# Kernel optimization log

Hardware: AMD Instinct MI355X
Metric: run time of the kernel (lower is better)

## Reference

```python
import jax, jax.numpy as jnp
import numpy as np

SEQ, B, N, F_IN = 128, 32, 1024, 16
NHID, G_FEAT, H = 2, 4, 256


def setup_inputs() -> dict:
    key = jax.random.key(0)
    ks = jax.random.split(key, 14)
    inp = {}
    inp['x'] = jax.random.normal(ks[0], (SEQ, B, N, F_IN), jnp.float32)
    # row-scaled random dense adjacency (keeps activations well-conditioned)
    inp['adj'] = jax.random.uniform(ks[1], (N, N), jnp.float32) * (1.0 / N)
    inp['gc1_w'] = jax.random.normal(ks[2], (F_IN, NHID), jnp.float32) * 0.3
    inp['gc1_b'] = jax.random.normal(ks[3], (NHID,), jnp.float32) * 0.1
    inp['gc2_w'] = jax.random.normal(ks[4], (NHID, G_FEAT), jnp.float32) * 0.3
    inp['gc2_b'] = jax.random.normal(ks[5], (G_FEAT,), jnp.float32) * 0.1
    in0 = G_FEAT * N  # GRU layer-0 input size = G_feat * num_nodes
    inp['w_ih_l0'] = jax.random.normal(ks[6], (3 * H, in0), jnp.float32) * 0.02
    inp['w_hh_l0'] = jax.random.normal(ks[7], (3 * H, H), jnp.float32) * 0.05
    inp['b_ih_l0'] = jax.random.normal(ks[8], (3 * H,), jnp.float32) * 0.05
    inp['b_hh_l0'] = jax.random.normal(ks[9], (3 * H,), jnp.float32) * 0.05
    inp['w_ih_l1'] = jax.random.normal(ks[10], (3 * H, H), jnp.float32) * 0.05
    inp['w_hh_l1'] = jax.random.normal(ks[11], (3 * H, H), jnp.float32) * 0.05
    inp['b_ih_l1'] = jax.random.normal(ks[12], (3 * H,), jnp.float32) * 0.05
    inp['b_hh_l1'] = jax.random.normal(ks[13], (3 * H,), jnp.float32) * 0.05
    return inp


def gru_layer(x_seq, h0, w_ih, w_hh, b_ih, b_hh):
    # torch nn.GRU gate math, gate order (r, z, n)
    def step(h, x_t):
        gi = x_t @ w_ih.T + b_ih          # (B, 3H)
        gh = h @ w_hh.T + b_hh            # (B, 3H)
        i_r, i_z, i_n = jnp.split(gi, 3, axis=-1)
        h_r, h_z, h_n = jnp.split(gh, 3, axis=-1)
        r = jax.nn.sigmoid(i_r + h_r)
        z = jax.nn.sigmoid(i_z + h_z)
        n = jnp.tanh(i_n + r * h_n)
        h_new = (1.0 - z) * n + z * h
        return h_new, h_new
    hT, out = jax.lax.scan(step, h0, x_seq)
    return out, hT


def reference(x, adj, gc1_w, gc1_b, gc2_w, gc2_b,
              w_ih_l0, w_hh_l0, b_ih_l0, b_hh_l0,
              w_ih_l1, w_hh_l1, b_ih_l1, b_hh_l1):
    # GCN, vectorized over (seq, batch). GraphConvolution: adj @ (x @ W) + b
    s = jnp.einsum('sbnf,fh->sbnh', x, gc1_w) + gc1_b
    s = jnp.einsum('mn,sbnh->sbmh', adj, s)
    s = jax.nn.relu(s)
    # dropout inactive in eval mode
    s = jnp.einsum('sbnh,hg->sbng', s, gc2_w) + gc2_b
    s = jnp.einsum('mn,sbng->sbmg', adj, s)
    s = jax.nn.log_softmax(s, axis=2)  # dim=1 of per-step (B, N, G) == node axis
    out = s.reshape(SEQ, B, N * G_FEAT)  # .view(batch, -1) per step, stacked
    h0 = jnp.zeros((B, H), out.dtype)
    out, h1 = gru_layer(out, h0, w_ih_l0, w_hh_l0, b_ih_l0, b_hh_l0)
    out, h2 = gru_layer(out, h0, w_ih_l1, w_hh_l1, b_ih_l1, b_hh_l1)
    hn = jnp.stack([h1, h2])  # (n_layers, B, H)
    return out, hn
```

## Files before the change

### kernel.cpp

```cpp
#include <hip/hip_runtime.h>
#include <stdint.h>

constexpr int SEQL = 128;
constexpr int BAT  = 32;
constexpr int NN   = 1024;
constexpr int FIN  = 16;
constexpr int HH   = 256;
constexpr int PQ   = SEQL * BAT;
constexpr float LSM_SHIFT = 6.9314718055994531f;

using f32x4 = __attribute__((ext_vector_type(4))) float;
using s16x8 = __attribute__((ext_vector_type(8))) short;
using u32x4 = __attribute__((ext_vector_type(4))) unsigned int;

__device__ __forceinline__ unsigned short f2bf(float x) {
  unsigned u = __float_as_uint(x);
  u += 0x7fffu + ((u >> 16) & 1u);
  return (unsigned short)(u >> 16);
}
__device__ __forceinline__ float sigm(float x) { return 1.f / (1.f + __expf(-x)); }

__device__ __forceinline__ void gl_lds16(const void* g, void* l) {
  __builtin_amdgcn_global_load_lds(
      (const __attribute__((address_space(1))) void*)g,
      (__attribute__((address_space(3))) void*)l, 16, 0, 0);
}

#if __has_builtin(__builtin_amdgcn_fdot2_f32_bf16)
typedef __bf16 bf16x2_t __attribute__((ext_vector_type(2)));
__device__ __forceinline__ float dot2bf(unsigned w, unsigned h, float acc) {
  return __builtin_amdgcn_fdot2_f32_bf16(__builtin_bit_cast(bf16x2_t, w),
                                         __builtin_bit_cast(bf16x2_t, h), acc, false);
}
#else
__device__ __forceinline__ float dot2bf(unsigned w, unsigned h, float acc) {
  acc += __uint_as_float(w << 16) * __uint_as_float(h << 16);
  acc += __uint_as_float(w & 0xffff0000u) * __uint_as_float(h & 0xffff0000u);
  return acc;
}
#endif

__global__ __launch_bounds__(256) void k1_xw1(const float* __restrict__ x,
    const float* __restrict__ w1, const float* __restrict__ b1,
    unsigned short* __restrict__ Yt) {
  int idx = blockIdx.x * 256 + threadIdx.x;
  int p = idx >> 10, n = idx & 1023;
  const float* xp = x + (size_t)idx * FIN;
  float xv[16];
  *(float4*)(xv + 0)  = *(const float4*)(xp + 0);
  *(float4*)(xv + 4)  = *(const float4*)(xp + 4);
  *(float4*)(xv + 8)  = *(const float4*)(xp + 8);
  *(float4*)(xv + 12) = *(const float4*)(xp + 12);
  float y0 = b1[0], y1 = b1[1];
#pragma unroll
  for (int f = 0; f < 16; ++f) { y0 += xv[f] * w1[2*f]; y1 += xv[f] * w1[2*f+1]; }
  Yt[(size_t)(2*p)   * NN + n] = f2bf(y0);
  Yt[(size_t)(2*p+1) * NN + n] = f2bf(y1);
}

__global__ __launch_bounds__(256) void k_cvt(const float* __restrict__ in,
    unsigned short* __restrict__ out, int n4) {
  int i = blockIdx.x * 256 + threadIdx.x;
  if (i >= n4) return;
  float4 v = *(const float4*)(in + (size_t)i * 4);
  ushort4 o;
  o.x = f2bf(v.x); o.y = f2bf(v.y); o.z = f2bf(v.z); o.w = f2bf(v.w);
  *(ushort4*)(out + (size_t)i * 4) = o;
}

__global__ __launch_bounds__(256) void k_biasadj(const float* __restrict__ wih0,
    const float* __restrict__ bih0, float* __restrict__ biasAdj) {
  int wid = threadIdx.x >> 6, lane = threadIdx.x & 63;
  int j = blockIdx.x * 4 + wid;
  const float* row = wih0 + (size_t)j * 4096;
  float s = 0.f;
  for (int k = lane * 4; k < 4096; k += 256) {
    float4 v = *(const float4*)(row + k);
    s += v.x + v.y + v.z + v.w;
  }
#pragma unroll
  for (int off = 32; off >= 1; off >>= 1) s += __shfl_xor(s, off);
  if (lane == 0) biasAdj[j] = bih0[j] - LSM_SHIFT * s;
}

template <int KS>
__global__ __launch_bounds__(256) void k_prep(const float* __restrict__ W,
    unsigned* __restrict__ Wp) {
  int tid = blockIdx.x * 256 + threadIdx.x;
  int j = tid >> 7, k2 = tid & 127;
  float2 wv = *(const float2*)(W + (size_t)j * 256 + 2 * k2);
  unsigned pk = (unsigned)f2bf(wv.x) | ((unsigned)f2bf(wv.y) << 16);
  int i = j >> 8, jg = j & 255;
  if (KS == 4) {
    int kg = k2 >> 5, c = (k2 >> 2) & 7, u = k2 & 3;
    Wp[(((i * 4 + kg) * 8 + c) << 10) + (jg << 2) + u] = pk;
  } else {
    int kg = k2 >> 6, c = (k2 >> 2) & 15, u = k2 & 3;
    Wp[(((i * 2 + kg) * 16 + c) << 10) + (jg << 2) + u] = pk;
  }
}

template <int EPI>
__global__ __launch_bounds__(256) void gemm_bt(
    const unsigned short* __restrict__ A, const unsigned short* __restrict__ B,
    void* __restrict__ Cout, const float* __restrict__ bias, int K, int ldc) {
  __shared__ __align__(16) unsigned short As[128 * 64];
  __shared__ __align__(16) unsigned short Bs[128 * 64];
  const int tid = threadIdx.x;
  const int lane = tid & 63, wave = tid >> 6;
  const int ln15 = lane & 15, hi4 = lane >> 4;
  const int wr = wave >> 1, wc = wave & 1;
  const int m0 = blockIdx.y * 128, n0 = blockIdx.x * 128;
  const int rsub = lane >> 3, csub = lane & 7;

  f32x4 acc[4][4];
#pragma unroll
  for (int i = 0; i < 4; ++i)
#pragma unroll
    for (int j = 0; j < 4; ++j) acc[i][j] = {0.f, 0.f, 0.f, 0.f};

  for (int kt = 0; kt < K; kt += 64) {
    __syncthreads();
#pragma unroll
    for (int j = 0; j < 4; ++j) {
      int qq = wave * 4 + j;
      const unsigned short* ga = A + (size_t)(m0 + qq*8 + rsub) * K + kt + csub*8;
      gl_lds16(ga, &As[qq * 512]);
      const unsigned short* gb = B + (size_t)(n0 + qq*8 + rsub) * K + kt + csub*8;
      gl_lds16(gb, &Bs[qq * 512]);
    }
    __syncthreads();
#pragma unroll
    for (int kk = 0; kk < 2; ++kk) {
      s16x8 af[4], bfr[4];
#pragma unroll
      for (int mi = 0; mi < 4; ++mi)
        af[mi] = *(const s16x8*)&As[(wr*64 + mi*16 + ln15) * 64 + kk*32 + hi4*8];
#pragma unroll
      for (int ni = 0; ni < 4; ++ni)
        bfr[ni] = *(const s16x8*)&Bs[(wc*64 + ni*16 + ln15) * 64 + kk*32 + hi4*8];
#pragma unroll
      for (int mi = 0; mi < 4; ++mi)
#pragma unroll
        for (int ni = 0; ni < 4; ++ni)
          acc[mi][ni] = __builtin_amdgcn_mfma_f32_16x16x32_bf16(
              af[mi], bfr[ni], acc[mi][ni], 0, 0, 0);
    }
  }

  if (EPI == 2) {
    float* C = (float*)Cout;
#pragma unroll
    for (int ni = 0; ni < 4; ++ni) {
      int j = n0 + wc*64 + ni*16 + ln15;
      float bv = bias[j];
#pragma unroll
      for (int mi = 0; mi < 4; ++mi) {
        int m = m0 + wr*64 + mi*16 + hi4*4;
#pragma unroll
        for (int r = 0; r < 4; ++r) C[(size_t)(m + r) * ldc + j] = acc[mi][ni][r] + bv;
      }
    }
  } else {
    unsigned short* C = (unsigned short*)Cout;
#pragma unroll
    for (int ni = 0; ni < 4; ++ni) {
      int j = n0 + wc*64 + ni*16 + ln15;
#pragma unroll
      for (int mi = 0; mi < 4; ++mi) {
        int m = m0 + wr*64 + mi*16 + hi4*4;
        ushort4 v;
        float f0 = acc[mi][ni][0], f1 = acc[mi][ni][1], f2 = acc[mi][ni][2], f3 = acc[mi][ni][3];
        if (EPI == 0) { f0 = fmaxf(f0, 0.f); f1 = fmaxf(f1, 0.f); f2 = fmaxf(f2, 0.f); f3 = fmaxf(f3, 0.f); }
        v.x = f2bf(f0); v.y = f2bf(f1); v.z = f2bf(f2); v.w = f2bf(f3);
        *(ushort4*)&C[(size_t)j * ldc + m] = v;
      }
    }
  }
}

__device__ __forceinline__ unsigned k4_proc(unsigned a, unsigned b, float w0, float w1, float bb) {
  float a0 = __uint_as_float(a << 16), a1 = __uint_as_float(a & 0xffff0000u);
  float b0 = __uint_as_float(b << 16), b1 = __uint_as_float(b & 0xffff0000u);
  float y0 = a0 * w0 + b0 * w1 + bb;
  float y1 = a1 * w0 + b1 * w1 + bb;
  return (unsigned)f2bf(y0) | ((unsigned)f2bf(y1) << 16);
}

__global__ __launch_bounds__(256) void k4_w2(const unsigned short* __restrict__ z1t,
    const float* __restrict__ w2, const float* __restrict__ b2,
    unsigned short* __restrict__ Y2t) {
  int idx = blockIdx.x * 256 + threadIdx.x;
  int j4 = idx >> 7, mb = idx & 127;
  int p = j4 >> 2, g = j4 & 3;
  const unsigned short* r0 = z1t + (size_t)(p * 2) * NN + mb * 8;
  const unsigned short* r1 = r0 + NN;
  float w0 = w2[g], w1v = w2[4 + g], bb = b2[g];
  uint4 ua = *(const uint4*)r0;
  uint4 ub = *(const uint4*)r1;
  uint4 o;
  o.x = k4_proc(ua.x, ub.x, w0, w1v, bb);
  o.y = k4_proc(ua.y, ub.y, w0, w1v, bb);
  o.z = k4_proc(ua.z, ub.z, w0, w1v, bb);
  o.w = k4_proc(ua.w, ub.w, w0, w1v, bb);
  *(uint4*)(Y2t + (size_t)j4 * NN + mb * 8) = o;
}

__global__ __launch_bounds__(256) void k6_lsm(const unsigned short* __restrict__ z2t,
    unsigned short* __restrict__ Xg) {
  int wid = threadIdx.x >> 6, lane = threadIdx.x & 63;
  int r = blockIdx.x * 4 + wid;
  int p = r >> 2, g = r & 3;
  const unsigned short* row = z2t + (size_t)r * NN;
  uint4 u0 = *(const uint4*)(row + lane * 16);
  uint4 u1 = *(const uint4*)(row + lane * 16 + 8);
  unsigned uu[8] = {u0.x, u0.y, u0.z, u0.w, u1.x, u1.y, u1.z, u1.w};
  float v[16];
#pragma unroll
  for (int q = 0; q < 8; ++q) {
    v[2*q]   = __uint_as_float(uu[q] << 16);
    v[2*q+1] = __uint_as_float(uu[q] & 0xffff0000u);
  }
  float mx = v[0];
#pragma unroll
  for (int e = 1; e < 16; ++e) mx = fmaxf(mx, v[e]);
#pragma unroll
  for (int off = 32; off >= 1; off >>= 1) mx = fmaxf(mx, __shfl_xor(mx, off));
  float s = 0.f;
#pragma unroll
  for (int e = 0; e < 16; ++e) s += __expf(v[e] - mx);
#pragma unroll
  for (int off = 32; off >= 1; off >>= 1) s += __shfl_xor(s, off);
  float lse = __logf(s) + mx;
  unsigned short* xr = Xg + (size_t)p * 4096;
#pragma unroll
  for (int e = 0; e < 16; ++e) xr[(lane * 16 + e) * 4 + g] = f2bf(v[e] - lse + LSM_SHIFT);
}

template <int L>
__global__ __attribute__((amdgpu_flat_work_group_size(1024, 1024),
                          amdgpu_waves_per_eu(4, 4)))
void k_rnn4(const float* __restrict__ gi,
    const unsigned* __restrict__ Wp, const float* __restrict__ bhh,
    unsigned short* __restrict__ hb_out, float* __restrict__ hf_out,
    float* __restrict__ hn_row) {
  const int b = blockIdx.x, tid = threadIdx.x;
  const int jg = tid & 255, kg = tid >> 8;
  __shared__ __align__(16) unsigned hpk[128];
  __shared__ float part[4][776];

  unsigned w[3][8][4];
#pragma unroll
  for (int i = 0; i < 3; ++i)
#pragma unroll
    for (int c = 0; c < 8; ++c) {
      u32x4 t = *(const u32x4*)(Wp + ((((i * 4 + kg) * 8 + c) << 10) + (jg << 2)));
      w[i][c][0] = t.x; w[i][c][1] = t.y; w[i][c][2] = t.z; w[i][c][3] = t.w;
#pragma unroll
      for (int u = 0; u < 4; ++u) asm volatile("" : "+v"(w[i][c][u]));
    }

  float hprev = 0.f;
  float br = 0.f, bz = 0.f, bn = 0.f;
  float g0 = 0.f, g1 = 0.f, g2 = 0.f;
  if (tid < 256) {
    br = bhh[jg]; bz = bhh[256 + jg]; bn = bhh[512 + jg];
    const float* gr = gi + (size_t)b * 768;
    g0 = gr[jg]; g1 = gr[256 + jg]; g2 = gr[512 + jg];
  }
  if (tid < 128) hpk[tid] = 0u;
  __syncthreads();

  for (int t = 0; t < SEQL; ++t) {
    float p0 = 0.f, p1 = 0.f, p2 = 0.f;
    if (tid < 256) {
      int tt = t + 1 < SEQL ? t + 1 : SEQL - 1;
      const float* gr = gi + (size_t)(tt * BAT + b) * 768;
      p0 = gr[jg]; p1 = gr[256 + jg]; p2 = gr[512 + jg];
    }
    float a0 = 0.f, a1 = 0.f, a2 = 0.f;
    u32x4 hk = *(const u32x4*)&hpk[kg * 32];
#pragma unroll
    for (int c = 0; c < 8; ++c) {
      u32x4 hnx = (c < 7) ? *(const u32x4*)&hpk[kg * 32 + (c + 1) * 4] : hk;
      a0 = dot2bf(w[0][c][0], hk.x, a0); a0 = dot2bf(w[0][c][1], hk.y, a0);
      a0 = dot2bf(w[0][c][2], hk.z, a0); a0 = dot2bf(w[0][c][3], hk.w, a0);
      a1 = dot2bf(w[1][c][0], hk.x, a1); a1 = dot2bf(w[1][c][1], hk.y, a1);
      a1 = dot2bf(w[1][c][2], hk.z, a1); a1 = dot2bf(w[1][c][3], hk.w, a1);
      a2 = dot2bf(w[2][c][0], hk.x, a2); a2 = dot2bf(w[2][c][1], hk.y, a2);
      a2 = dot2bf(w[2][c][2], hk.z, a2); a2 = dot2bf(w[2][c][3], hk.w, a2);
      hk = hnx;
    }
    part[kg][jg]       = a0;
    part[kg][256 + jg] = a1;
    part[kg][512 + jg] = a2;
    __syncthreads();
    if (tid < 256) {
      float ghr = part[0][jg]       + part[1][jg]       + part[2][jg]       + part[3][jg]       + br;
      float ghz = part[0][256 + jg] + part[1][256 + jg] + part[2][256 + jg] + part[3][256 + jg] + bz;
      float ghn = part[0][512 + jg] + part[1][512 + jg] + part[2][512 + jg] + part[3][512 + jg] + bn;
      float r = sigm(g0 + ghr);
      float z = sigm(g1 + ghz);
      float nn = tanhf(g2 + r * ghn);
      float hnew = (1.f - z) * nn + z * hprev;
      hprev = hnew;
      unsigned short hbb = f2bf(hnew);
      if (L == 0) hb_out[(size_t)(t * BAT + b) * 256 + jg] = hbb;
      else        hf_out[(size_t)(t * BAT + b) * 256 + jg] = hnew;
      unsigned lo = (unsigned)hbb;
      unsigned hi = (unsigned)__shfl_down((int)lo, 1);
      if (!(jg & 1)) hpk[jg >> 1] = lo | (hi << 16);
      if (t == SEQL - 1) hn_row[b * 256 + jg] = hnew;
    }
    g0 = p0; g1 = p1; g2 = p2;
    __syncthreads();
  }
}

template <int L>
__global__ __attribute__((amdgpu_flat_work_group_size(512, 512),
                          amdgpu_waves_per_eu(2, 2)))
void k_rnn2(const float* __restrict__ gi,
    const unsigned* __restrict__ Wp, const float* __restrict__ bhh,
    unsigned short* __restrict__ hb_out, float* __restrict__ hf_out,
    float* __restrict__ hn_row) {
  const int b = blockIdx.x, tid = threadIdx.x;
  const int jg = tid & 255, kg = tid >> 8;
  __shared__ __align__(16) unsigned hpk[128];
  __shared__ float part[2][776];

  unsigned w[3][16][4];
#pragma unroll
  for (int i = 0; i < 3; ++i)
#pragma unroll
    for (int c = 0; c < 16; ++c) {
      u32x4 t = *(const u32x4*)(Wp + ((((i * 2 + kg) * 16 + c) << 10) + (jg << 2)));
      w[i][c][0] = t.x; w[i][c][1] = t.y; w[i][c][2] = t.z; w[i][c][3] = t.w;
#pragma unroll
      for (int u = 0; u < 4; ++u) asm volatile("" : "+v"(w[i][c][u]));
    }

  float hprev = 0.f;
  float br = 0.f, bz = 0.f, bn = 0.f;
  float g0 = 0.f, g1 = 0.f, g2 = 0.f;
  if (tid < 256) {
    br = bhh[jg]; bz = bhh[256 + jg]; bn = bhh[512 + jg];
    const float* gr = gi + (size_t)b * 768;
    g0 = gr[jg]; g1 = gr[256 + jg]; g2 = gr[512 + jg];
  }
  if (tid < 128) hpk[tid] = 0u;
  __syncthreads();

  for (int t = 0; t < SEQL; ++t) {
    float p0 = 0.f, p1 = 0.f, p2 = 0.f;
    if (tid < 256) {
      int tt = t + 1 < SEQL ? t + 1 : SEQL - 1;
      const float* gr = gi + (size_t)(tt * BAT + b) * 768;
      p0 = gr[jg]; p1 = gr[256 + jg]; p2 = gr[512 + jg];
    }
    float a0 = 0.f, a1 = 0.f, a2 = 0.f;
#pragma unroll
    for (int c = 0; c < 16; ++c) {
      u32x4 hk = *(const u32x4*)&hpk[kg * 64 + c * 4];
      a0 = dot2bf(w[0][c][0], hk.x, a0); a0 = dot2bf(w[0][c][1], hk.y, a0);
      a0 = dot2bf(w[0][c][2], hk.z, a0); a0 = dot2bf(w[0][c][3], hk.w, a0);
      a1 = dot2bf(w[1][c][0], hk.x, a1); a1 = dot2bf(w[1][c][1], hk.y, a1);
      a1 = dot2bf(w[1][c][2], hk.z, a1); a1 = dot2bf(w[1][c][3], hk.w, a1);
      a2 = dot2bf(w[2][c][0], hk.x, a2); a2 = dot2bf(w[2][c][1], hk.y, a2);
      a2 = dot2bf(w[2][c][2], hk.z, a2); a2 = dot2bf(w[2][c][3], hk.w, a2);
    }
    part[kg][jg]       = a0;
    part[kg][256 + jg] = a1;
    part[kg][512 + jg] = a2;
    __syncthreads();
    if (tid < 256) {
      float ghr = part[0][jg]       + part[1][jg]       + br;
      float ghz = part[0][256 + jg] + part[1][256 + jg] + bz;
      float ghn = part[0][512 + jg] + part[1][512 + jg] + bn;
      float r = sigm(g0 + ghr);
      float z = sigm(g1 + ghz);
      float nn = tanhf(g2 + r * ghn);
      float hnew = (1.f - z) * nn + z * hprev;
      hprev = hnew;
      unsigned short hbb = f2bf(hnew);
      if (L == 0) hb_out[(size_t)(t * BAT + b) * 256 + jg] = hbb;
      else        hf_out[(size_t)(t * BAT + b) * 256 + jg] = hnew;
      unsigned lo = (unsigned)hbb;
      unsigned hi = (unsigned)__shfl_down((int)lo, 1);
      if (!(jg & 1)) hpk[jg >> 1] = lo | (hi << 16);
      if (t == SEQL - 1) hn_row[b * 256 + jg] = hnew;
    }
    g0 = p0; g1 = p1; g2 = p2;
    __syncthreads();
  }
}

extern "C" void kernel_launch(void* const* d_in, const int* in_sizes, int n_in,
                              void* d_out, int out_size, void* d_ws, size_t ws_size,
                              hipStream_t stream) {
  const float* x    = (const float*)d_in[0];
  const float* adj  = (const float*)d_in[1];
  const float* gc1w = (const float*)d_in[2];
  const float* gc1b = (const float*)d_in[3];
  const float* gc2w = (const float*)d_in[4];
  const float* gc2b = (const float*)d_in[5];
  const float* wih0 = (const float*)d_in[6];
  const float* whh0 = (const float*)d_in[7];
  const float* bih0 = (const float*)d_in[8];
  const float* bhh0 = (const float*)d_in[9];
  const float* wih1 = (const float*)d_in[10];
  const float* whh1 = (const float*)d_in[11];
  const float* bih1 = (const float*)d_in[12];
  const float* bhh1 = (const float*)d_in[13];

  char* ws = (char*)d_ws;
  const size_t MB = 1048576;
  unsigned short* adjb  = (unsigned short*)(ws + 0);
  unsigned short* Yt    = (unsigned short*)(ws + 2 * MB);
  unsigned short* z1t   = (unsigned short*)(ws + 18 * MB);
  unsigned short* Y2t   = (unsigned short*)(ws + 34 * MB);
  unsigned short* z2t   = (unsigned short*)(ws + 2 * MB);
  unsigned short* Xg    = (unsigned short*)(ws + 34 * MB);
  unsigned short* wih0b = (unsigned short*)(ws + 2 * MB);
  float* biasAdj        = (float*)(ws + 9 * MB);
  float* gi0            = (float*)(ws + 10 * MB);
  unsigned* Whh0p       = (unsigned*)(ws + 23 * MB);
  unsigned* Whh1p       = (unsigned*)(ws + 24 * MB);
  unsigned short* wih1b = (unsigned short*)(ws + 25 * MB);
  unsigned short* h0b   = (unsigned short*)(ws + 25 * MB + 512 * 1024);
  float* gi1            = (float*)(ws + 28 * MB);
  float* out = (float*)d_out;
  float* hn  = out + (size_t)SEQL * BAT * HH;

  k1_xw1<<<PQ * NN / 256, 256, 0, stream>>>(x, gc1w, gc1b, Yt);
  k_cvt<<<(NN * NN / 4 + 255) / 256, 256, 0, stream>>>(adj, adjb, NN * NN / 4);
  gemm_bt<0><<<dim3(64, 8), 256, 0, stream>>>(adjb, Yt, (void*)z1t, nullptr, 1024, 1024);
  k4_w2<<<16384 * 128 / 256, 256, 0, stream>>>(z1t, gc2w, gc2b, Y2t);
  gemm_bt<1><<<dim3(128, 8), 256, 0, stream>>>(adjb, Y2t, (void*)z2t, nullptr, 1024, 1024);
  k6_lsm<<<16384 / 4, 256, 0, stream>>>(z2t, Xg);
  k_biasadj<<<192, 256, 0, stream>>>(wih0, bih0, biasAdj);
  k_cvt<<<(768 * 4096 / 4 + 255) / 256, 256, 0, stream>>>(wih0, wih0b, 768 * 4096 / 4);
  gemm_bt<2><<<dim3(6, 32), 256, 0, stream>>>(Xg, wih0b, (void*)gi0, biasAdj, 4096, 768);
  k_prep<4><<<384, 256, 0, stream>>>(whh0, Whh0p);
  k_prep<2><<<384, 256, 0, stream>>>(whh1, Whh1p);
  k_cvt<<<(768 * 256 / 4 + 255) / 256, 256, 0, stream>>>(wih1, wih1b, 768 * 256 / 4);
  k_rnn4<0><<<32, 1024, 0, stream>>>(gi0, Whh0p, bhh0, h0b, nullptr, hn);
  gemm_bt<2><<<dim3(6, 32), 256, 0, stream>>>(h0b, wih1b, (void*)gi1, bih1, 256, 768);
  k_rnn2<1><<<32, 512, 0, stream>>>(gi1, Whh1p, bhh1, nullptr, out, hn + BAT * HH);
}
```

Measured before the change: 714.2 us.

## Switch layer-0 GRU recurrence to 512-thread blocks with vector-register weight tiles

Layer-0 recurrent kernel now uses 512 threads (2 k-groups) instead of 1024 (4 k-groups). Each thread holds 192 packed bf16 weight words in six 32-wide vector registers, with a matching new prepacking layout. Layer 1 also drops its waves_per_eu attribute in favour of launch_bounds(512,1). The goal is to cut partial-sum reduction and barrier cost per timestep. The cost is twice the dot-product work per thread and heavy register pressure that may cause spills.

```diff
diff --git a/kernel.cpp b/kernel.cpp
--- a/kernel.cpp
+++ b/kernel.cpp
@@ -12,6 +12,7 @@
 using f32x4 = __attribute__((ext_vector_type(4))) float;
 using s16x8 = __attribute__((ext_vector_type(8))) short;
 using u32x4 = __attribute__((ext_vector_type(4))) unsigned int;
+using u32x32 = __attribute__((ext_vector_type(32))) unsigned int;
 
 __device__ __forceinline__ unsigned short f2bf(float x) {
   unsigned u = __float_as_uint(x);
@@ -83,21 +84,26 @@
   if (lane == 0) biasAdj[j] = bih0[j] - LSM_SHIFT * s;
 }
 
-template <int KS>
-__global__ __launch_bounds__(256) void k_prep(const float* __restrict__ W,
+__global__ __launch_bounds__(256) void k_prepT(const float* __restrict__ W,
     unsigned* __restrict__ Wp) {
   int tid = blockIdx.x * 256 + threadIdx.x;
   int j = tid >> 7, k2 = tid & 127;
   float2 wv = *(const float2*)(W + (size_t)j * 256 + 2 * k2);
   unsigned pk = (unsigned)f2bf(wv.x) | ((unsigned)f2bf(wv.y) << 16);
-  int i = j >> 8, jg = j & 255;
-  if (KS == 4) {
-    int kg = k2 >> 5, c = (k2 >> 2) & 7, u = k2 & 3;
-    Wp[(((i * 4 + kg) * 8 + c) << 10) + (jg << 2) + u] = pk;
-  } else {
-    int kg = k2 >> 6, c = (k2 >> 2) & 15, u = k2 & 3;
-    Wp[(((i * 2 + kg) * 16 + c) << 10) + (jg << 2) + u] = pk;
-  }
+  int i = j >> 8, jg = j & 255, kg = k2 >> 6;
+  int r = k2 & 63, c = r >> 2, u = r & 3;
+  int t6 = i * 2 + (c >> 3), e = (c & 7) * 4 + u;
+  Wp[(((size_t)(t6 * 2 + kg) * 256 + jg) << 5) + e] = pk;
+}
+
+__global__ __launch_bounds__(256) void k_prep2(const float* __restrict__ W,
+    unsigned* __restrict__ Wp) {
+  int tid = blockIdx.x * 256 + threadIdx.x;
+  int j = tid >> 7, k2 = tid & 127;
+  float2 wv = *(const float2*)(W + (size_t)j * 256 + 2 * k2);
+  unsigned pk = (unsigned)f2bf(wv.x) | ((unsigned)f2bf(wv.y) << 16);
+  int i = j >> 8, jg = j & 255, kg = k2 >> 6, c = (k2 >> 2) & 15, u = k2 & 3;
+  Wp[(((i * 2 + kg) * 16 + c) << 10) + (jg << 2) + u] = pk;
 }
 
 template <int EPI>
@@ -238,27 +244,26 @@
 }
 
 template <int L>
-__global__ __attribute__((amdgpu_flat_work_group_size(1024, 1024),
-                          amdgpu_waves_per_eu(4, 4)))
-void k_rnn4(const float* __restrict__ gi,
+__global__ __launch_bounds__(512, 1) void k_rnnT(const float* __restrict__ gi,
     const unsigned* __restrict__ Wp, const float* __restrict__ bhh,
     unsigned short* __restrict__ hb_out, float* __restrict__ hf_out,
     float* __restrict__ hn_row) {
   const int b = blockIdx.x, tid = threadIdx.x;
   const int jg = tid & 255, kg = tid >> 8;
   __shared__ __align__(16) unsigned hpk[128];
-  __shared__ float part[4][776];
-
-  unsigned w[3][8][4];
-#pragma unroll
-  for (int i = 0; i < 3; ++i)
-#pragma unroll
-    for (int c = 0; c < 8; ++c) {
-      u32x4 t = *(const u32x4*)(Wp + ((((i * 4 + kg) * 8 + c) << 10) + (jg << 2)));
-      w[i][c][0] = t.x; w[i][c][1] = t.y; w[i][c][2] = t.z; w[i][c][3] = t.w;
-#pragma unroll
-      for (int u = 0; u < 4; ++u) asm volatile("" : "+v"(w[i][c][u]));
-    }
+  __shared__ float part[2][776];
+
+  u32x32 W6[6];
+#pragma unroll
+  for (int t6 = 0; t6 < 6; ++t6) {
+    const u32x4* src = (const u32x4*)(Wp + (((size_t)(t6 * 2 + kg) * 256 + jg) << 5));
+#pragma unroll
+    for (int q = 0; q < 8; ++q) {
+      u32x4 v = src[q];
+      W6[t6][q * 4 + 0] = v.x; W6[t6][q * 4 + 1] = v.y;
+      W6[t6][q * 4 + 2] = v.z; W6[t6][q * 4 + 3] = v.w;
+    }
+  }
 
   float hprev = 0.f;
   float br = 0.f, bz = 0.f, bn = 0.f;
@@ -279,26 +284,31 @@
       p0 = gr[jg]; p1 = gr[256 + jg]; p2 = gr[512 + jg];
     }
     float a0 = 0.f, a1 = 0.f, a2 = 0.f;
-    u32x4 hk = *(const u32x4*)&hpk[kg * 32];
-#pragma unroll
-    for (int c = 0; c < 8; ++c) {
-      u32x4 hnx = (c < 7) ? *(const u32x4*)&hpk[kg * 32 + (c + 1) * 4] : hk;
-      a0 = dot2bf(w[0][c][0], hk.x, a0); a0 = dot2bf(w[0][c][1], hk.y, a0);
-      a0 = dot2bf(w[0][c][2], hk.z, a0); a0 = dot2bf(w[0][c][3], hk.w, a0);
-      a1 = dot2bf(w[1][c][0], hk.x, a1); a1 = dot2bf(w[1][c][1], hk.y, a1);
-      a1 = dot2bf(w[1][c][2], hk.z, a1); a1 = dot2bf(w[1][c][3], hk.w, a1);
-      a2 = dot2bf(w[2][c][0], hk.x, a2); a2 = dot2bf(w[2][c][1], hk.y, a2);
-      a2 = dot2bf(w[2][c][2], hk.z, a2); a2 = dot2bf(w[2][c][3], hk.w, a2);
-      hk = hnx;
+#pragma unroll
+    for (int c = 0; c < 16; ++c) {
+      u32x4 hk = *(const u32x4*)&hpk[kg * 64 + c * 4];
+      const int hi = c >> 3, eb = (c & 7) * 4;
+      a0 = dot2bf(W6[0 + hi][eb + 0], hk.x, a0);
+      a0 = dot2bf(W6[0 + hi][eb + 1], hk.y, a0);
+      a0 = dot2bf(W6[0 + hi][eb + 2], hk.z, a0);
+      a0 = dot2bf(W6[0 + hi][eb + 3], hk.w, a0);
+      a1 = dot2bf(W6[2 + hi][eb + 0], hk.x, a1);
+      a1 = dot2bf(W6[2 + hi][eb + 1], hk.y, a1);
+      a1 = dot2bf(W6[2 + hi][eb + 2], hk.z, a1);
+      a1 = dot2bf(W6[2 + hi][eb + 3], hk.w, a1);
+      a2 = dot2bf(W6[4 + hi][eb + 0], hk.x, a2);
+      a2 = dot2bf(W6[4 + hi][eb + 1], hk.y, a2);
+      a2 = dot2bf(W6[4 + hi][eb + 2], hk.z, a2);
+      a2 = dot2bf(W6[4 + hi][eb + 3], hk.w, a2);
     }
     part[kg][jg]       = a0;
     part[kg][256 + jg] = a1;
     part[kg][512 + jg] = a2;
     __syncthreads();
     if (tid < 256) {
-      float ghr = part[0][jg]       + part[1][jg]       + part[2][jg]       + part[3][jg]       + br;
-      float ghz = part[0][256 + jg] + part[1][256 + jg] + part[2][256 + jg] + part[3][256 + jg] + bz;
-      float ghn = part[0][512 + jg] + part[1][512 + jg] + part[2][512 + jg] + part[3][512 + jg] + bn;
+      float ghr = part[0][jg]       + part[1][jg]       + br;
+      float ghz = part[0][256 + jg] + part[1][256 + jg] + bz;
+      float ghn = part[0][512 + jg] + part[1][512 + jg] + bn;
       float r = sigm(g0 + ghr);
       float z = sigm(g1 + ghz);
       float nn = tanhf(g2 + r * ghn);
@@ -308,8 +318,8 @@
       if (L == 0) hb_out[(size_t)(t * BAT + b) * 256 + jg] = hbb;
       else        hf_out[(size_t)(t * BAT + b) * 256 + jg] = hnew;
       unsigned lo = (unsigned)hbb;
-      unsigned hi = (unsigned)__shfl_down((int)lo, 1);
-      if (!(jg & 1)) hpk[jg >> 1] = lo | (hi << 16);
+      unsigned hi2 = (unsigned)__shfl_down((int)lo, 1);
+      if (!(jg & 1)) hpk[jg >> 1] = lo | (hi2 << 16);
       if (t == SEQL - 1) hn_row[b * 256 + jg] = hnew;
     }
     g0 = p0; g1 = p1; g2 = p2;
@@ -318,9 +328,7 @@
 }
 
 template <int L>
-__global__ __attribute__((amdgpu_flat_work_group_size(512, 512),
-                          amdgpu_waves_per_eu(2, 2)))
-void k_rnn2(const float* __restrict__ gi,
+__global__ __launch_bounds__(512, 1) void k_rnn5(const float* __restrict__ gi,
     const unsigned* __restrict__ Wp, const float* __restrict__ bhh,
     unsigned short* __restrict__ hb_out, float* __restrict__ hf_out,
     float* __restrict__ hn_row) {
@@ -441,10 +449,10 @@
   k_biasadj<<<192, 256, 0, stream>>>(wih0, bih0, biasAdj);
   k_cvt<<<(768 * 4096 / 4 + 255) / 256, 256, 0, stream>>>(wih0, wih0b, 768 * 4096 / 4);
   gemm_bt<2><<<dim3(6, 32), 256, 0, stream>>>(Xg, wih0b, (void*)gi0, biasAdj, 4096, 768);
-  k_prep<4><<<384, 256, 0, stream>>>(whh0, Whh0p);
-  k_prep<2><<<384, 256, 0, stream>>>(whh1, Whh1p);
+  k_prepT<<<384, 256, 0, stream>>>(whh0, Whh0p);
+  k_prep2<<<384, 256, 0, stream>>>(whh1, Whh1p);
   k_cvt<<<(768 * 256 / 4 + 255) / 256, 256, 0, stream>>>(wih1, wih1b, 768 * 256 / 4);
-  k_rnn4<0><<<32, 1024, 0, stream>>>(gi0, Whh0p, bhh0, h0b, nullptr, hn);
+  k_rnnT<0><<<32, 512, 0, stream>>>(gi0, Whh0p, bhh0, h0b, nullptr, hn);
   gemm_bt<2><<<dim3(6, 32), 256, 0, stream>>>(h0b, wih1b, (void*)gi1, bih1, 256, 768);
-  k_rnn2<1><<<32, 512, 0, stream>>>(gi1, Whh1p, bhh1, nullptr, out, hn + BAT * HH);
-}
+  k_rnn5<1><<<32, 512, 0, stream>>>(gi1, Whh1p, bhh1, nullptr, out, hn + BAT * HH);
+}
```

Result: faster. 672.0 us (-5.9%).
